# Optimization experiments

Hardware: AMD Instinct MI355X
Metric: run time of the kernel (lower is better)

Reference implementation:

```python
import jax, jax.numpy as jnp
import numpy as np

B, M, S, D, Q, H = 8, 8192, 128, 512, 32, 8
HD = D // H
LN_EPS = 1e-5


def setup_inputs() -> dict:
    key = jax.random.key(0)
    ks = jax.random.split(key, 12)
    inp = {
        "memory": jax.random.normal(ks[0], (B, M, D), dtype=jnp.float32),
        "context": jax.random.normal(ks[1], (B, S, D), dtype=jnp.float32),
        "memory_mask": jax.random.randint(ks[2], (B, M), 0, 2).astype(bool),
        # learned parameters
        "queries_param": jax.random.normal(ks[3], (Q, D), dtype=jnp.float32) * 0.02,
        "ctx_w": jax.random.normal(ks[4], (D, D), dtype=jnp.float32) / np.sqrt(D),
        "ctx_b": jnp.zeros((D,), dtype=jnp.float32),
        "in_w": jax.random.normal(ks[5], (3 * D, D), dtype=jnp.float32) / np.sqrt(D),
        "in_b": jnp.zeros((3 * D,), dtype=jnp.float32),
        "out_w": jax.random.normal(ks[6], (D, D), dtype=jnp.float32) / np.sqrt(D),
        "out_b": jnp.zeros((D,), dtype=jnp.float32),
        "ln_g": jnp.ones((D,), dtype=jnp.float32),
        "ln_b": jnp.zeros((D,), dtype=jnp.float32),
        "gate_w": jax.random.normal(ks[7], (Q, D), dtype=jnp.float32) / np.sqrt(D),
        "gate_b": jnp.zeros((Q,), dtype=jnp.float32),
    }
    return inp


def _forward(memory, context, memory_mask, queries_param, ctx_w, ctx_b,
             in_w, in_b, out_w, out_b, ln_g, ln_b, gate_w, gate_b):
    b = memory.shape[0]
    # pool context over sequence dim (rank-3 path)
    pooled = context.mean(axis=1)  # [B, D]
    # queries + projected context
    queries = queries_param[None, :, :] + (pooled @ ctx_w.T + ctx_b)[:, None, :]  # [B, Q, D]
    # MultiheadAttention in-projection
    wq, wk, wv = in_w[:D], in_w[D:2 * D], in_w[2 * D:]
    bq, bk, bv = in_b[:D], in_b[D:2 * D], in_b[2 * D:]
    qh = (queries @ wq.T + bq).reshape(b, Q, H, HD).transpose(0, 2, 1, 3)   # [B,H,Q,hd]
    kh = (memory @ wk.T + bk).reshape(b, M, H, HD).transpose(0, 2, 1, 3)    # [B,H,M,hd]
    vh = (memory @ wv.T + bv).reshape(b, M, H, HD).transpose(0, 2, 1, 3)    # [B,H,M,hd]
    scale = 1.0 / np.sqrt(HD)
    scores = jnp.einsum('bhqd,bhkd->bhqk', qh * scale, kh)                  # [B,H,Q,M]
    # key_padding_mask: True in memory_mask means valid; invalid -> -inf
    scores = jnp.where(memory_mask[:, None, None, :], scores, -jnp.inf)
    attn = jax.nn.softmax(scores, axis=-1)                                   # [B,H,Q,M]
    ctx_out = jnp.einsum('bhqk,bhkd->bhqd', attn, vh)
    ctx_out = ctx_out.transpose(0, 2, 1, 3).reshape(b, Q, D)
    readouts = ctx_out @ out_w.T + out_b                                     # [B,Q,D]
    attention = attn.mean(axis=1)                                            # [B,Q,M]
    gates = jax.nn.sigmoid(pooled @ gate_w.T + gate_b)                       # [B,Q]
    readouts = readouts * gates[:, :, None]
    mu = readouts.mean(axis=-1, keepdims=True)
    var = readouts.var(axis=-1, keepdims=True)
    readouts_norm = (readouts - mu) * jax.lax.rsqrt(var + LN_EPS) * ln_g + ln_b
    return readouts_norm, attention, gates, queries


def reference(memory, context, memory_mask, queries_param, ctx_w, ctx_b,
              in_w, in_b, out_w, out_b, ln_g, ln_b, gate_w, gate_b):
    return _forward(memory, context, memory_mask, queries_param, ctx_w, ctx_b,
                    in_w, in_b, out_w, out_b, ln_g, ln_b, gate_w, gate_b)
```

## Files before the change

### kernel.cpp

```cpp
#include <hip/hip_runtime.h>
#include <cstdint>

#define BB 8
#define MM 8192
#define SS 128
#define DD 512
#define QQ 32
#define HH 8
#define HDD 64
#define LN_EPS 1e-5f

typedef __bf16 bf16;
typedef _Float16 f16;
typedef __attribute__((ext_vector_type(8))) __bf16 bf16x8;
typedef __attribute__((ext_vector_type(4))) __bf16 bf16x4;
typedef __attribute__((ext_vector_type(8))) _Float16 f16x8;
typedef __attribute__((ext_vector_type(4))) float f32x4;

#define NEG_INF (-__builtin_inff())

__global__ __launch_bounds__(512) void k_front(const float* __restrict__ ctx,
                                               const float* __restrict__ ctx_w,
                                               const float* __restrict__ ctx_b,
                                               const float* __restrict__ qp,
                                               const float* __restrict__ gate_w,
                                               const float* __restrict__ gate_b,
                                               float* __restrict__ q_out,
                                               float* __restrict__ gates_out) {
    __shared__ float pl[DD];
    __shared__ float scratch[512];
    __shared__ float proj[64];
    int blk = blockIdx.x;
    int b = blk >> 3, js = blk & 7;
    int t = threadIdx.x;
    const float* p = ctx + (size_t)b * SS * DD + t;
    float s = 0.f;
#pragma unroll 8
    for (int i = 0; i < SS; i++) s += p[(size_t)i * DD];
    pl[t] = s * (1.0f / SS);
    __syncthreads();
    int r = js * 64 + (t & 63), ks = t >> 6;
    {
        const f32x4* wr = (const f32x4*)(ctx_w + (size_t)r * DD + ks * 64);
        const f32x4* pv = (const f32x4*)(pl + ks * 64);
        float a = 0.f;
#pragma unroll
        for (int k = 0; k < 16; k++) {
            f32x4 w = wr[k], pp = pv[k];
            a += w.x * pp.x + w.y * pp.y + w.z * pp.z + w.w * pp.w;
        }
        scratch[t] = a;
    }
    __syncthreads();
    if (t < 64) {
        float sum = ctx_b[js * 64 + t];
#pragma unroll
        for (int s8 = 0; s8 < 8; s8++) sum += scratch[t + 64 * s8];
        proj[t] = sum;
    }
    __syncthreads();
    int col = js * 64 + (t & 63);
    float pr = proj[t & 63];
#pragma unroll
    for (int qq = 0; qq < 4; qq++) {
        int q = (t >> 6) * 4 + qq;
        q_out[((size_t)(b * QQ + q)) * DD + col] = qp[q * DD + col] + pr;
    }
    if (js == 0 && t < QQ) {
        const f32x4* gw = (const f32x4*)(gate_w + (size_t)t * DD);
        const f32x4* pv = (const f32x4*)pl;
        float ga = 0.f;
#pragma unroll 8
        for (int k = 0; k < DD / 4; k++) {
            f32x4 w = gw[k], pp = pv[k];
            ga += w.x * pp.x + w.y * pp.y + w.z * pp.z + w.w * pp.w;
        }
        gates_out[b * QQ + t] = 1.0f / (1.0f + __expf(-(ga + gate_b[t])));
    }
}

__global__ __launch_bounds__(256) void k_qh(const float* __restrict__ q_in,
                                            const float* __restrict__ in_w,
                                            const float* __restrict__ in_b,
                                            float* __restrict__ qh) {
    __shared__ float qr[QQ * DD];
    int blk = blockIdx.x;
    int b = blk >> 3, js = blk & 7;
    int t = threadIdx.x;
    const f32x4* src = (const f32x4*)(q_in + (size_t)b * QQ * DD);
    f32x4* dst = (f32x4*)qr;
    for (int i = t; i < QQ * DD / 4; i += 256) dst[i] = src[i];
    __syncthreads();
    int j = js * 64 + (t & 63);
    int qg = t >> 6;
    const f32x4* wv = (const f32x4*)(in_w + (size_t)j * DD);
    float acc[8];
#pragma unroll
    for (int e = 0; e < 8; e++) acc[e] = 0.f;
    for (int k = 0; k < DD / 4; k++) {
        f32x4 w = wv[k];
#pragma unroll
        for (int e = 0; e < 8; e++) {
            f32x4 qq = ((const f32x4*)qr)[(qg * 8 + e) * (DD / 4) + k];
            acc[e] += w.x * qq.x + w.y * qq.y + w.z * qq.z + w.w * qq.w;
        }
    }
    float bias = in_b[j];
#pragma unroll
    for (int e = 0; e < 8; e++) {
        int q = qg * 8 + e;
        qh[((size_t)(b * QQ + q)) * DD + j] = 0.125f * (acc[e] + bias);
    }
}

__global__ void k_cvt(const float* __restrict__ src, bf16* __restrict__ dst, int n4) {
    int i = blockIdx.x * blockDim.x + threadIdx.x;
    if (i >= n4) return;
    f32x4 v = ((const f32x4*)src)[i];
    bf16x4 o;
    o.x = (bf16)v.x; o.y = (bf16)v.y; o.z = (bf16)v.z; o.w = (bf16)v.w;
    ((bf16x4*)dst)[i] = o;
}

#define GLOAD(gp, lp)                                                                   \
    __builtin_amdgcn_global_load_lds((const __attribute__((address_space(1))) void*)(gp), \
                                     (__attribute__((address_space(3))) void*)(lp), 16, 0, 0)

__global__ __launch_bounds__(512, 2) void k_gemm_kv(const bf16* __restrict__ A,
                                                    const bf16* __restrict__ Bw,
                                                    const float* __restrict__ in_b,
                                                    bf16* __restrict__ Kh,
                                                    bf16* __restrict__ Vt) {
    __shared__ __align__(16) bf16 sm[65536];
    const int tid = threadIdx.x;
    const int w = tid >> 6, l = tid & 63;
    const int wm = w >> 2, wn = w & 3;
    const int lq = l & 15, quad = l >> 4, lx = l & 7;
    const int lr = l >> 3, gc = (l & 7) ^ lr;
    const int sb = (w >> 1) * 8 + (w & 1) * 2;

    const int bid = blockIdx.x;
    const int swz = (bid & 7) * 128 + (bid >> 3);
    const int bm = swz >> 2, bn = swz & 3;

    const bf16* aPtr = A + (size_t)(bm * 256 + w * 8 + lr) * 512 + gc * 8;
    const bf16* bPtr = Bw + (size_t)(bn * 256 + sb * 8 + lr) * 512 + gc * 8;

#pragma unroll
    for (int p = 0; p < 4; p++) GLOAD(aPtr + p * 32768, sm + (p * 8 + w) * 512);
#pragma unroll
    for (int p = 0; p < 4; p++) {
        GLOAD(bPtr + ((p & 1) * 8 + (p >> 1) * 32) * 512,
              sm + 16384 + (sb + (p & 1) + (p >> 1) * 4) * 512);
        if (p == 1) __builtin_amdgcn_sched_barrier(0);
    }
    aPtr += 64;
    bPtr += 64;

    const f32x4 vzero = {0.f, 0.f, 0.f, 0.f};
    f32x4 acc[8][4];
#pragma unroll
    for (int i = 0; i < 8; i++)
#pragma unroll
        for (int j = 0; j < 4; j++) acc[i][j] = vzero;

#pragma unroll
    for (int T = 0; T < 8; T++) {
        bf16* Ab = sm + (T & 1) * 32768;
        bf16* Bb = Ab + 16384;
        bf16* AbN = sm + ((T + 1) & 1) * 32768;
        bf16* BbN = AbN + 16384;
        const bool pf = (T < 7);

        asm volatile("s_waitcnt vmcnt(2)" ::: "memory");
        __builtin_amdgcn_s_barrier();
        bf16x8 af[8][2], b01[2][2];
        {
            const int c0 = (quad ^ lx) << 3;
#pragma unroll
            for (int i = 0; i < 8; i++) {
                const bf16* rp = Ab + (wm * 128 + i * 16 + lq) * 64;
                af[i][0] = *(const bf16x8*)(rp + c0);
                af[i][1] = *(const bf16x8*)(rp + (c0 ^ 32));
            }
#pragma unroll
            for (int j = 0; j < 2; j++) {
                const bf16* rp = Bb + (wn * 64 + j * 16 + lq) * 64;
                b01[j][0] = *(const bf16x8*)(rp + c0);
                b01[j][1] = *(const bf16x8*)(rp + (c0 ^ 32));
            }
        }
        if (pf) {
#pragma unroll
            for (int p = 0; p < 4; p++) GLOAD(aPtr + p * 32768, AbN + (p * 8 + w) * 512);
            aPtr += 64;
        }
        __builtin_amdgcn_s_setprio(1);
#pragma unroll
        for (int i = 0; i < 8; i++)
#pragma unroll
            for (int j = 0; j < 2; j++) {
                acc[i][j] = __builtin_amdgcn_mfma_f32_16x16x32_bf16(af[i][0], b01[j][0], acc[i][j], 0, 0, 0);
                acc[i][j] = __builtin_amdgcn_mfma_f32_16x16x32_bf16(af[i][1], b01[j][1], acc[i][j], 0, 0, 0);
            }
        __builtin_amdgcn_s_setprio(0);

        if (pf) {
            asm volatile("s_waitcnt vmcnt(4)" ::: "memory");
        } else {
            asm volatile("s_waitcnt vmcnt(0)" ::: "memory");
        }
        __builtin_amdgcn_s_barrier();
        bf16x8 b23[2][2];
        {
            const int c0 = (quad ^ lx) << 3;
#pragma unroll
            for (int j = 0; j < 2; j++) {
                const bf16* rp = Bb + (wn * 64 + 32 + j * 16 + lq) * 64;
                b23[j][0] = *(const bf16x8*)(rp + c0);
                b23[j][1] = *(const bf16x8*)(rp + (c0 ^ 32));
            }
        }
        if (pf) {
#pragma unroll
            for (int p = 0; p < 4; p++) {
                GLOAD(bPtr + ((p & 1) * 8 + (p >> 1) * 32) * 512,
                      BbN + (sb + (p & 1) + (p >> 1) * 4) * 512);
                if (p == 1) __builtin_amdgcn_sched_barrier(0);
            }
            bPtr += 64;
        }
        __builtin_amdgcn_s_setprio(1);
#pragma unroll
        for (int i = 0; i < 8; i++)
#pragma unroll
            for (int j = 0; j < 2; j++) {
                acc[i][2 + j] = __builtin_amdgcn_mfma_f32_16x16x32_bf16(af[i][0], b23[j][0], acc[i][2 + j], 0, 0, 0);
                acc[i][2 + j] = __builtin_amdgcn_mfma_f32_16x16x32_bf16(af[i][1], b23[j][1], acc[i][2 + j], 0, 0, 0);
            }
        __builtin_amdgcn_s_setprio(0);
    }

    __syncthreads();
    const int qn_w = wn >> 1;
    bf16* qt = sm + (((wm << 1) | qn_w) * 16384);
    const bool isV = (bn >= 2);
    if (!isV) {
#pragma unroll
        for (int j = 0; j < 4; j++) {
            int cq = (wn & 1) * 64 + j * 16 + lq;
            float bias = in_b[512 + bn * 256 + qn_w * 128 + cq];
            int cc = cq >> 3, cl = cq & 7;
#pragma unroll
            for (int i = 0; i < 8; i++) {
                int rb = i * 16 + quad * 4;
#pragma unroll
                for (int t = 0; t < 4; t++) {
                    int r = rb + t;
                    qt[r * 128 + (((cc ^ (r & 15)) << 3) | cl)] = (bf16)(acc[i][j][t] + bias);
                }
            }
        }
        __syncthreads();
        for (int idx = tid; idx < 8192; idx += 512) {
            int qq2 = idx >> 11;
            int rr = (idx >> 4) & 127, ch2 = idx & 15;
            bf16x8 v = *(const bf16x8*)(sm + qq2 * 16384 + rr * 128 + ((ch2 ^ (rr & 15)) << 3));
            int m = bm * 256 + (qq2 >> 1) * 128 + rr;
            int cg = bn * 256 + (qq2 & 1) * 128 + ch2 * 8;
            int b = m >> 13, mloc = m & 8191;
            int h = cg >> 6, d = cg & 63;
            *(bf16x8*)(Kh + (((size_t)(b * 8 + h) * 8192 + mloc) << 6) + d) = v;
        }
    } else {
#pragma unroll
        for (int j = 0; j < 4; j++) {
            int cq = (wn & 1) * 64 + j * 16 + lq;
            float bias = in_b[512 + bn * 256 + qn_w * 128 + cq];
            int cs = cq & 15;
#pragma unroll
            for (int i = 0; i < 8; i++) {
                int rb = i * 16 + quad * 4;
#pragma unroll
                for (int t = 0; t < 4; t++) {
                    int r = rb + t;
                    qt[cq * 128 + ((((r >> 3) ^ cs) << 3) | (r & 7))] = (bf16)(acc[i][j][t] + bias);
                }
            }
        }
        __syncthreads();
        for (int idx = tid; idx < 8192; idx += 512) {
            int qq2 = idx >> 11;
            int cq = (idx >> 4) & 127, ch2 = idx & 15;
            bf16x8 v = *(const bf16x8*)(sm + qq2 * 16384 + cq * 128 + ((ch2 ^ (cq & 15)) << 3));
            int hd = (bn - 2) * 256 + (qq2 & 1) * 128 + cq;
            int m = bm * 256 + (qq2 >> 1) * 128 + ch2 * 8;
            int b = m >> 13, mloc = m & 8191;
            *(bf16x8*)(Vt + ((size_t)(b * 512 + hd)) * MM + mloc) = v;
        }
    }
}
#undef GLOAD

__global__ __launch_bounds__(256) void k_scores(const float* __restrict__ qh,
                                                const bf16* __restrict__ kvK,
                                                const int* __restrict__ mask,
                                                f16* __restrict__ s16,
                                                float* __restrict__ statsM,
                                                float* __restrict__ statsS) {
    __shared__ __align__(16) f16 tile[QQ * 528];
    __shared__ float smx[QQ][4];
    __shared__ float sse[QQ][4];
    __shared__ float qmax[QQ];
    int blk = blockIdx.x;
    int mt = blk & 15, h = (blk >> 4) & 7, b = blk >> 7;
    int tid = threadIdx.x, w = tid >> 6, l = tid & 63;
    int lq = l & 15, quad = l >> 4;
    int mbase = mt * 512 + w * 128;

    bf16x8 af[2][2];
#pragma unroll
    for (int i = 0; i < 2; i++)
#pragma unroll
        for (int s = 0; s < 2; s++) {
            const float* qp = qh + ((size_t)(b * QQ + i * 16 + lq)) * DD + h * 64 + s * 32 + quad * 8;
            f32x4 q0 = *(const f32x4*)qp;
            f32x4 q1 = *(const f32x4*)(qp + 4);
            bf16x8 v;
            v[0] = (bf16)q0.x; v[1] = (bf16)q0.y; v[2] = (bf16)q0.z; v[3] = (bf16)q0.w;
            v[4] = (bf16)q1.x; v[5] = (bf16)q1.y; v[6] = (bf16)q1.z; v[7] = (bf16)q1.w;
            af[i][s] = v;
        }

    const f32x4 vzero = {0.f, 0.f, 0.f, 0.f};
    f32x4 acc[2][8];
#pragma unroll
    for (int i = 0; i < 2; i++)
#pragma unroll
        for (int n = 0; n < 8; n++) acc[i][n] = vzero;

#pragma unroll
    for (int n = 0; n < 8; n++) {
        int m = mbase + n * 16 + lq;
        const bf16* kp = kvK + (((size_t)(b * HH + h) * MM + m) << 6) + quad * 8;
        bf16x8 b0 = *(const bf16x8*)kp;
        bf16x8 b1 = *(const bf16x8*)(kp + 32);
#pragma unroll
        for (int i = 0; i < 2; i++) {
            acc[i][n] = __builtin_amdgcn_mfma_f32_16x16x32_bf16(af[i][0], b0, acc[i][n], 0, 0, 0);
            acc[i][n] = __builtin_amdgcn_mfma_f32_16x16x32_bf16(af[i][1], b1, acc[i][n], 0, 0, 0);
        }
    }
#pragma unroll
    for (int n = 0; n < 8; n++) {
        int mv = mask[b * MM + mbase + n * 16 + lq];
        if (!mv) {
#pragma unroll
            for (int i = 0; i < 2; i++)
#pragma unroll
                for (int t = 0; t < 4; t++) acc[i][n][t] = NEG_INF;
        }
    }
    float mx[2][4];
#pragma unroll
    for (int i = 0; i < 2; i++)
#pragma unroll
        for (int t = 0; t < 4; t++) {
            float m = acc[i][0][t];
#pragma unroll
            for (int n = 1; n < 8; n++) m = fmaxf(m, acc[i][n][t]);
            mx[i][t] = m;
        }
#pragma unroll
    for (int off = 1; off < 16; off <<= 1)
#pragma unroll
        for (int i = 0; i < 2; i++)
#pragma unroll
            for (int t = 0; t < 4; t++) mx[i][t] = fmaxf(mx[i][t], __shfl_xor(mx[i][t], off, 64));
    if (lq == 0) {
#pragma unroll
        for (int i = 0; i < 2; i++)
#pragma unroll
            for (int t = 0; t < 4; t++) smx[i * 16 + quad * 4 + t][w] = mx[i][t];
    }
    __syncthreads();
    if (tid < QQ) qmax[tid] = fmaxf(fmaxf(smx[tid][0], smx[tid][1]), fmaxf(smx[tid][2], smx[tid][3]));
    __syncthreads();
    float se[2][4];
#pragma unroll
    for (int i = 0; i < 2; i++)
#pragma unroll
        for (int t = 0; t < 4; t++) {
            float qm = qmax[i * 16 + quad * 4 + t];
            float s = 0.f;
#pragma unroll
            for (int n = 0; n < 8; n++) s += __expf(acc[i][n][t] - qm);
            se[i][t] = s;
        }
#pragma unroll
    for (int off = 1; off < 16; off <<= 1)
#pragma unroll
        for (int i = 0; i < 2; i++)
#pragma unroll
            for (int t = 0; t < 4; t++) se[i][t] += __shfl_xor(se[i][t], off, 64);
    if (lq == 0) {
#pragma unroll
        for (int i = 0; i < 2; i++)
#pragma unroll
            for (int t = 0; t < 4; t++) sse[i * 16 + quad * 4 + t][w] = se[i][t];
    }
#pragma unroll
    for (int n = 0; n < 8; n++) {
        int mloc = w * 128 + n * 16 + lq;
#pragma unroll
        for (int i = 0; i < 2; i++)
#pragma unroll
            for (int t = 0; t < 4; t++)
                tile[(i * 16 + quad * 4 + t) * 528 + mloc] = (f16)acc[i][n][t];
    }
    __syncthreads();
    if (tid < QQ) {
        statsM[(size_t)blk * QQ + tid] = qmax[tid];
        statsS[(size_t)blk * QQ + tid] = sse[tid][0] + sse[tid][1] + sse[tid][2] + sse[tid][3];
    }
    for (int it = tid; it < 2048; it += 256) {
        int q = it >> 6, c = it & 63;
        f16x8 v = *(const f16x8*)(tile + q * 528 + c * 8);
        *(f16x8*)(s16 + ((size_t)((b * HH + h) * QQ + q)) * MM + mt * 512 + c * 8) = v;
    }
}

__global__ __launch_bounds__(256) void k_attn(const f16* __restrict__ s16,
                                              const float* __restrict__ statsM,
                                              const float* __restrict__ statsS,
                                              float* __restrict__ attn_out) {
    __shared__ float cM[128], cS[128], Mh[HH], iLh[HH];
    int blk = blockIdx.x;
    int ms = blk & 3, q = (blk >> 2) & 31, b = blk >> 7;
    int t = threadIdx.x;
    if (t < 128) {
        int h = t >> 4, c = t & 15;
        size_t sidx = (size_t)(((b * HH + h) * 16 + c)) * QQ + q;
        cM[t] = statsM[sidx];
        cS[t] = statsS[sidx];
    }
    __syncthreads();
    if (t < HH) {
        float M = NEG_INF;
#pragma unroll
        for (int c = 0; c < 16; c++) M = fmaxf(M, cM[t * 16 + c]);
        float L = 0.f;
#pragma unroll
        for (int c = 0; c < 16; c++) L += cS[t * 16 + c] * __expf(cM[t * 16 + c] - M);
        Mh[t] = M;
        iLh[t] = (1.0f / L) * (1.0f / HH);
    }
    __syncthreads();
    int m0 = ms * 2048 + t * 8;
    float am[8];
#pragma unroll
    for (int e = 0; e < 8; e++) am[e] = 0.f;
#pragma unroll
    for (int h = 0; h < HH; h++) {
        f16x8 v = *(const f16x8*)(s16 + ((size_t)((b * HH + h) * QQ + q)) * MM + m0);
        float M = Mh[h], iL = iLh[h];
#pragma unroll
        for (int e = 0; e < 8; e++) am[e] += __expf((float)v[e] - M) * iL;
    }
    float* ao = attn_out + (size_t)(b * QQ + q) * MM + m0;
    f32x4 o0 = {am[0], am[1], am[2], am[3]};
    f32x4 o1 = {am[4], am[5], am[6], am[7]};
    *(f32x4*)ao = o0;
    *(f32x4*)(ao + 4) = o1;
}

__global__ __launch_bounds__(256) void k_pv(const f16* __restrict__ s16,
                                            const float* __restrict__ statsM,
                                            const float* __restrict__ statsS,
                                            const bf16* __restrict__ Vt,
                                            float* __restrict__ ctxo_p) {
    __shared__ float ctile[QQ * HDD];
    __shared__ float Mq[QQ], iLq[QQ];
    int blk = blockIdx.x;
    int ck = blk & 7, h = (blk >> 3) & 7, b = blk >> 6;
    int t = threadIdx.x, w = t >> 6, l = t & 63;
    int lq = l & 15, quad = l >> 4;
    if (t < QQ) {
        const float* pM = statsM + (size_t)((b * HH + h) * 16) * QQ + t;
        const float* pS = statsS + (size_t)((b * HH + h) * 16) * QQ + t;
        float M = NEG_INF;
#pragma unroll
        for (int c = 0; c < 16; c++) M = fmaxf(M, pM[c * QQ]);
        float L = 0.f;
#pragma unroll
        for (int c = 0; c < 16; c++) L += pS[c * QQ] * __expf(pM[c * QQ] - M);
        Mq[t] = M;
        iLq[t] = 1.0f / L;
    }
    __syncthreads();
    int m0 = ck * 1024 + w * 256;

    const f16* P0 = s16 + ((size_t)((b * HH + h) * QQ + lq)) * MM + m0 + quad * 8;
    const f16* P1 = P0 + (size_t)16 * MM;
    const bf16* Vrow = Vt + ((size_t)((b * HH + h) * HDD + lq)) * MM + m0 + quad * 8;
    float M0 = Mq[lq], iL0 = iLq[lq];
    float M1 = Mq[16 + lq], iL1 = iLq[16 + lq];

    const f32x4 vzero = {0.f, 0.f, 0.f, 0.f};
    f32x4 acc[2][4];
#pragma unroll
    for (int i = 0; i < 2; i++)
#pragma unroll
        for (int j = 0; j < 4; j++) acc[i][j] = vzero;

#pragma unroll 2
    for (int ks = 0; ks < 256; ks += 32) {
        f16x8 r0 = *(const f16x8*)(P0 + ks);
        f16x8 r1 = *(const f16x8*)(P1 + ks);
        bf16x8 a0, a1;
#pragma unroll
        for (int e = 0; e < 8; e++) a0[e] = (bf16)(__expf((float)r0[e] - M0) * iL0);
#pragma unroll
        for (int e = 0; e < 8; e++) a1[e] = (bf16)(__expf((float)r1[e] - M1) * iL1);
        bf16x8 bv[4];
#pragma unroll
        for (int j = 0; j < 4; j++) bv[j] = *(const bf16x8*)(Vrow + (size_t)j * 16 * MM + ks);
#pragma unroll
        for (int j = 0; j < 4; j++) {
            acc[0][j] = __builtin_amdgcn_mfma_f32_16x16x32_bf16(a0, bv[j], acc[0][j], 0, 0, 0);
            acc[1][j] = __builtin_amdgcn_mfma_f32_16x16x32_bf16(a1, bv[j], acc[1][j], 0, 0, 0);
        }
    }
    for (int i = t; i < QQ * HDD; i += 256) ctile[i] = 0.f;
    __syncthreads();
#pragma unroll
    for (int i = 0; i < 2; i++)
#pragma unroll
        for (int j = 0; j < 4; j++)
#pragma unroll
            for (int tt = 0; tt < 4; tt++) {
                int q = i * 16 + quad * 4 + tt;
                int d = j * 16 + lq;
                atomicAdd(&ctile[q * HDD + d], acc[i][j][tt]);
            }
    __syncthreads();
    float* dst = ctxo_p + (size_t)ck * (BB * QQ * DD);
    for (int i = t; i < QQ * HDD; i += 256) {
        int q = i >> 6, d = i & 63;
        dst[((size_t)(b * QQ + q)) * DD + h * HDD + d] = ctile[i];
    }
}

__global__ __launch_bounds__(256) void k_outln(const float* __restrict__ ctxo_p,
                                               const float* __restrict__ out_w,
                                               const float* __restrict__ out_b,
                                               const float* __restrict__ gates,
                                               const float* __restrict__ ln_g,
                                               const float* __restrict__ ln_b,
                                               float* __restrict__ out0) {
    __shared__ float cr[DD];
    __shared__ float sred[4], sred2[4];
    int bq = blockIdx.x, t = threadIdx.x;
    float c0 = 0.f, c1 = 0.f;
#pragma unroll
    for (int c = 0; c < 8; c++) {
        const float* src = ctxo_p + (size_t)c * (BB * QQ * DD) + (size_t)bq * DD;
        c0 += src[t];
        c1 += src[t + 256];
    }
    cr[t] = c0;
    cr[t + 256] = c1;
    __syncthreads();
    float g = gates[bq];
    const f32x4* cv = (const f32x4*)cr;
    float r[2];
#pragma unroll
    for (int jj = 0; jj < 2; jj++) {
        int j = t + jj * 256;
        const f32x4* wv = (const f32x4*)(out_w + (size_t)j * DD);
        float acc = 0.f;
#pragma unroll 4
        for (int k = 0; k < DD / 4; k++) {
            f32x4 wq = wv[k], cq = cv[k];
            acc += wq.x * cq.x + wq.y * cq.y + wq.z * cq.z + wq.w * cq.w;
        }
        r[jj] = (acc + out_b[j]) * g;
    }
    float s1 = r[0] + r[1];
    float s2 = r[0] * r[0] + r[1] * r[1];
    for (int off = 32; off; off >>= 1) {
        s1 += __shfl_xor(s1, off, 64);
        s2 += __shfl_xor(s2, off, 64);
    }
    int wid = t >> 6;
    if ((t & 63) == 0) { sred[wid] = s1; sred2[wid] = s2; }
    __syncthreads();
    float S1 = sred[0] + sred[1] + sred[2] + sred[3];
    float S2 = sred2[0] + sred2[1] + sred2[2] + sred2[3];
    float mu = S1 * (1.0f / DD);
    float var = S2 * (1.0f / DD) - mu * mu;
    float rs = rsqrtf(var + LN_EPS);
#pragma unroll
    for (int jj = 0; jj < 2; jj++) {
        int j = t + jj * 256;
        out0[(size_t)bq * DD + j] = (r[jj] - mu) * rs * ln_g[j] + ln_b[j];
    }
}

extern "C" void kernel_launch(void* const* d_in, const int* in_sizes, int n_in,
                              void* d_out, int out_size, void* d_ws, size_t ws_size,
                              hipStream_t stream) {
    const float* memory  = (const float*)d_in[0];
    const float* context = (const float*)d_in[1];
    const int*   mask    = (const int*)d_in[2];
    const float* qp      = (const float*)d_in[3];
    const float* ctx_w   = (const float*)d_in[4];
    const float* ctx_b   = (const float*)d_in[5];
    const float* in_w    = (const float*)d_in[6];
    const float* in_b    = (const float*)d_in[7];
    const float* out_w   = (const float*)d_in[8];
    const float* out_b   = (const float*)d_in[9];
    const float* ln_g    = (const float*)d_in[10];
    const float* ln_b    = (const float*)d_in[11];
    const float* gate_w  = (const float*)d_in[12];
    const float* gate_b  = (const float*)d_in[13];

    float* out       = (float*)d_out;
    float* out_ln    = out;
    float* out_attn  = out + 131072;
    float* out_gates = out + 131072 + 2097152;
    float* out_q     = out_gates + 256;

    char* ws = (char*)d_ws;
    bf16*  memB   = (bf16*)ws;
    f16*   s16    = (f16*)ws;
    bf16*  kvK    = (bf16*)(ws + 67108864);
    bf16*  Vt     = (bf16*)(ws + 134217728);
    bf16*  kvwB   = (bf16*)(ws + 201326592);
    float* statsM = (float*)(ws + 201588736);
    float* statsS = (float*)(ws + 201719808);
    float* qh     = (float*)(ws + 202375168);
    float* ctxo_p = (float*)(ws + 202899456);

    k_front<<<64, 512, 0, stream>>>(context, ctx_w, ctx_b, qp, gate_w, gate_b, out_q, out_gates);
    k_qh<<<64, 256, 0, stream>>>(out_q, in_w, in_b, qh);
    k_cvt<<<32768, 256, 0, stream>>>(memory, memB, 8388608);
    k_cvt<<<512, 256, 0, stream>>>(in_w + 262144, kvwB, 131072);
    k_gemm_kv<<<1024, 512, 0, stream>>>(memB, kvwB, in_b, kvK, Vt);
    k_scores<<<1024, 256, 0, stream>>>(qh, kvK, mask, s16, statsM, statsS);
    k_attn<<<1024, 256, 0, stream>>>(s16, statsM, statsS, out_attn);
    k_pv<<<512, 256, 0, stream>>>(s16, statsM, statsS, Vt, ctxo_p);
    k_outln<<<BB * QQ, 256, 0, stream>>>(ctxo_p, out_w, out_b, out_gates, ln_g, ln_b, out_ln);
}
```

Measured before the change: 475.3 us.

## Fuse fp32-to-bf16 conversion of memory into the KV GEMM A-operand load

Drops the separate k_cvt pass over the 128 MB fp32 memory tensor. The KV GEMM now loads fp32 A tiles into registers, converts them to bf16 and writes them to LDS itself, software-pipelined two k-steps ahead, while B still uses direct global-to-LDS loads. This removes a full write and re-read of the bf16 copy. In exchange the GEMM reads twice as many bytes for A (once per N-tile block, four times in total), needs more registers at launch bounds 512x2, and adds VALU conversion work to the main loop.

```diff
diff --git a/kernel.cpp b/kernel.cpp
--- a/kernel.cpp
+++ b/kernel.cpp
@@ -125,8 +125,9 @@
 #define GLOAD(gp, lp)                                                                   \
     __builtin_amdgcn_global_load_lds((const __attribute__((address_space(1))) void*)(gp), \
                                      (__attribute__((address_space(3))) void*)(lp), 16, 0, 0)
-
-__global__ __launch_bounds__(512, 2) void k_gemm_kv(const bf16* __restrict__ A,
+#define SBAR0 __builtin_amdgcn_sched_barrier(0)
+
+__global__ __launch_bounds__(512, 2) void k_gemm_kv(const float* __restrict__ A32,
                                                     const bf16* __restrict__ Bw,
                                                     const float* __restrict__ in_b,
                                                     bf16* __restrict__ Kh,
@@ -143,26 +144,48 @@
     const int swz = (bid & 7) * 128 + (bid >> 3);
     const int bm = swz >> 2, bn = swz & 3;
 
-    const bf16* aPtr = A + (size_t)(bm * 256 + w * 8 + lr) * 512 + gc * 8;
-    const bf16* bPtr = Bw + (size_t)(bn * 256 + sb * 8 + lr) * 512 + gc * 8;
-
-#pragma unroll
-    for (int p = 0; p < 4; p++) GLOAD(aPtr + p * 32768, sm + (p * 8 + w) * 512);
-#pragma unroll
-    for (int p = 0; p < 4; p++) {
-        GLOAD(bPtr + ((p & 1) * 8 + (p >> 1) * 32) * 512,
-              sm + 16384 + (sb + (p & 1) + (p >> 1) * 4) * 512);
-        if (p == 1) __builtin_amdgcn_sched_barrier(0);
-    }
-    aPtr += 64;
-    bPtr += 64;
-
+    const float* aG = A32 + (size_t)(bm * 256 + w * 8 + lr) * 512 + (l & 7) * 8;
+    const int aWr = (w * 8 + lr) * 64 + gc * 8;
+    const bf16* bG = Bw + (size_t)(bn * 256 + sb * 8 + lr) * 512 + gc * 8;
+
+#define LOADA(ar, kk)                                                        \
+    _Pragma("unroll") for (int p = 0; p < 4; p++) {                          \
+        ar[p][0] = *(const f32x4*)(aG + (size_t)p * 32768 + (kk));           \
+        ar[p][1] = *(const f32x4*)(aG + (size_t)p * 32768 + (kk) + 4);       \
+    }
+#define WRITEA(buf, ar)                                                      \
+    _Pragma("unroll") for (int p = 0; p < 4; p++) {                          \
+        bf16x8 v_;                                                           \
+        v_[0] = (bf16)ar[p][0].x; v_[1] = (bf16)ar[p][0].y;                  \
+        v_[2] = (bf16)ar[p][0].z; v_[3] = (bf16)ar[p][0].w;                  \
+        v_[4] = (bf16)ar[p][1].x; v_[5] = (bf16)ar[p][1].y;                  \
+        v_[6] = (bf16)ar[p][1].z; v_[7] = (bf16)ar[p][1].w;                  \
+        *(bf16x8*)((buf) + aWr + p * 4096) = v_;                             \
+    }
+#define LOADB(buf, kk)                                                       \
+    _Pragma("unroll") for (int p = 0; p < 4; p++) {                          \
+        GLOAD(bG + (size_t)(((p & 1) * 8 + (p >> 1) * 32) * 512) + (kk),     \
+              (buf) + (sb + (p & 1) + (p >> 1) * 4) * 512);                  \
+    }
+
+    f32x4 aRegA[4][2], aRegB[4][2];
     const f32x4 vzero = {0.f, 0.f, 0.f, 0.f};
     f32x4 acc[8][4];
 #pragma unroll
     for (int i = 0; i < 8; i++)
 #pragma unroll
         for (int j = 0; j < 4; j++) acc[i][j] = vzero;
+
+    LOADA(aRegA, 0);
+    SBAR0;
+    LOADB(sm + 16384, 0);
+    SBAR0;
+    asm volatile("s_waitcnt vmcnt(4)" ::: "memory");
+    WRITEA(sm, aRegA);
+    LOADA(aRegB, 64);
+    SBAR0;
+    asm volatile("s_waitcnt vmcnt(8) lgkmcnt(0)" ::: "memory");
+    __builtin_amdgcn_s_barrier();
 
 #pragma unroll
     for (int T = 0; T < 8; T++) {
@@ -170,31 +193,23 @@
         bf16* Bb = Ab + 16384;
         bf16* AbN = sm + ((T + 1) & 1) * 32768;
         bf16* BbN = AbN + 16384;
-        const bool pf = (T < 7);
-
-        asm volatile("s_waitcnt vmcnt(2)" ::: "memory");
-        __builtin_amdgcn_s_barrier();
+        const int c0 = (quad ^ lx) << 3;
+
         bf16x8 af[8][2], b01[2][2];
-        {
-            const int c0 = (quad ^ lx) << 3;
-#pragma unroll
-            for (int i = 0; i < 8; i++) {
-                const bf16* rp = Ab + (wm * 128 + i * 16 + lq) * 64;
-                af[i][0] = *(const bf16x8*)(rp + c0);
-                af[i][1] = *(const bf16x8*)(rp + (c0 ^ 32));
-            }
-#pragma unroll
-            for (int j = 0; j < 2; j++) {
-                const bf16* rp = Bb + (wn * 64 + j * 16 + lq) * 64;
-                b01[j][0] = *(const bf16x8*)(rp + c0);
-                b01[j][1] = *(const bf16x8*)(rp + (c0 ^ 32));
-            }
-        }
-        if (pf) {
-#pragma unroll
-            for (int p = 0; p < 4; p++) GLOAD(aPtr + p * 32768, AbN + (p * 8 + w) * 512);
-            aPtr += 64;
-        }
+#pragma unroll
+        for (int i = 0; i < 8; i++) {
+            const bf16* rp = Ab + (wm * 128 + i * 16 + lq) * 64;
+            af[i][0] = *(const bf16x8*)(rp + c0);
+            af[i][1] = *(const bf16x8*)(rp + (c0 ^ 32));
+        }
+#pragma unroll
+        for (int j = 0; j < 2; j++) {
+            const bf16* rp = Bb + (wn * 64 + j * 16 + lq) * 64;
+            b01[j][0] = *(const bf16x8*)(rp + c0);
+            b01[j][1] = *(const bf16x8*)(rp + (c0 ^ 32));
+        }
+        asm volatile("s_waitcnt lgkmcnt(0)" ::: "memory");
+        SBAR0;
         __builtin_amdgcn_s_setprio(1);
 #pragma unroll
         for (int i = 0; i < 8; i++)
@@ -205,31 +220,28 @@
             }
         __builtin_amdgcn_s_setprio(0);
 
-        if (pf) {
+        if (T < 7) {
+            LOADB(BbN, (T + 1) * 64);
+            SBAR0;
             asm volatile("s_waitcnt vmcnt(4)" ::: "memory");
-        } else {
-            asm volatile("s_waitcnt vmcnt(0)" ::: "memory");
-        }
-        __builtin_amdgcn_s_barrier();
+            if ((T & 1) == 0) {
+                WRITEA(AbN, aRegB);
+                if (T < 6) LOADA(aRegA, (T + 2) * 64);
+            } else {
+                WRITEA(AbN, aRegA);
+                if (T < 6) LOADA(aRegB, (T + 2) * 64);
+            }
+            SBAR0;
+        }
         bf16x8 b23[2][2];
-        {
-            const int c0 = (quad ^ lx) << 3;
-#pragma unroll
-            for (int j = 0; j < 2; j++) {
-                const bf16* rp = Bb + (wn * 64 + 32 + j * 16 + lq) * 64;
-                b23[j][0] = *(const bf16x8*)(rp + c0);
-                b23[j][1] = *(const bf16x8*)(rp + (c0 ^ 32));
-            }
-        }
-        if (pf) {
-#pragma unroll
-            for (int p = 0; p < 4; p++) {
-                GLOAD(bPtr + ((p & 1) * 8 + (p >> 1) * 32) * 512,
-                      BbN + (sb + (p & 1) + (p >> 1) * 4) * 512);
-                if (p == 1) __builtin_amdgcn_sched_barrier(0);
-            }
-            bPtr += 64;
-        }
+#pragma unroll
+        for (int j = 0; j < 2; j++) {
+            const bf16* rp = Bb + (wn * 64 + 32 + j * 16 + lq) * 64;
+            b23[j][0] = *(const bf16x8*)(rp + c0);
+            b23[j][1] = *(const bf16x8*)(rp + (c0 ^ 32));
+        }
+        asm volatile("s_waitcnt lgkmcnt(0)" ::: "memory");
+        SBAR0;
         __builtin_amdgcn_s_setprio(1);
 #pragma unroll
         for (int i = 0; i < 8; i++)
@@ -239,7 +251,17 @@
                 acc[i][2 + j] = __builtin_amdgcn_mfma_f32_16x16x32_bf16(af[i][1], b23[j][1], acc[i][2 + j], 0, 0, 0);
             }
         __builtin_amdgcn_s_setprio(0);
-    }
+        if (T < 6) {
+            asm volatile("s_waitcnt vmcnt(8)" ::: "memory");
+            __builtin_amdgcn_s_barrier();
+        } else if (T == 6) {
+            asm volatile("s_waitcnt vmcnt(0)" ::: "memory");
+            __builtin_amdgcn_s_barrier();
+        }
+    }
+#undef LOADA
+#undef WRITEA
+#undef LOADB
 
     __syncthreads();
     const int qn_w = wn >> 1;
@@ -301,6 +323,7 @@
     }
 }
 #undef GLOAD
+#undef SBAR0
 
 __global__ __launch_bounds__(256) void k_scores(const float* __restrict__ qh,
                                                 const bf16* __restrict__ kvK,
@@ -632,7 +655,6 @@
     float* out_q     = out_gates + 256;
 
     char* ws = (char*)d_ws;
-    bf16*  memB   = (bf16*)ws;
     f16*   s16    = (f16*)ws;
     bf16*  kvK    = (bf16*)(ws + 67108864);
     bf16*  Vt     = (bf16*)(ws + 134217728);
@@ -644,9 +666,8 @@
 
     k_front<<<64, 512, 0, stream>>>(context, ctx_w, ctx_b, qp, gate_w, gate_b, out_q, out_gates);
     k_qh<<<64, 256, 0, stream>>>(out_q, in_w, in_b, qh);
-    k_cvt<<<32768, 256, 0, stream>>>(memory, memB, 8388608);
     k_cvt<<<512, 256, 0, stream>>>(in_w + 262144, kvwB, 131072);
-    k_gemm_kv<<<1024, 512, 0, stream>>>(memB, kvwB, in_b, kvK, Vt);
+    k_gemm_kv<<<1024, 512, 0, stream>>>(memory, kvwB, in_b, kvK, Vt);
     k_scores<<<1024, 256, 0, stream>>>(qh, kvK, mask, s16, statsM, statsS);
     k_attn<<<1024, 256, 0, stream>>>(s16, statsM, statsS, out_attn);
     k_pv<<<512, 256, 0, stream>>>(s16, statsM, statsS, Vt, ctxo_p);
```

Measured after the change: 693.3 us. 1.46x slower.

## Fuse P·V into the scores kernel with chunk-local softmax and rescale later

Applied to the files above, without the earlier changes.

The separate P·V kernel is removed. The scores kernel now computes exp(s - chunk_max) in place, stores these local probabilities as f16, and multiplies them against V (now stored as f16) with MFMA to write per-chunk partial context vectors. The output kernel and the attention-mean kernel rescale each chunk by exp(chunk_max - global_max)/L instead of recomputing exp per element. This removes a kernel launch and the re-read of the score matrix for P·V. In exchange it adds per-chunk partial buffers, more LDS and work in the scores kernel, and f16 precision for both V and the probabilities.

```diff
diff --git a/kernel.cpp b/kernel.cpp
--- a/kernel.cpp
+++ b/kernel.cpp
@@ -130,7 +130,7 @@
                                                     const bf16* __restrict__ Bw,
                                                     const float* __restrict__ in_b,
                                                     bf16* __restrict__ Kh,
-                                                    bf16* __restrict__ Vt) {
+                                                    f16* __restrict__ Vt) {
     __shared__ __align__(16) bf16 sm[65536];
     const int tid = threadIdx.x;
     const int w = tid >> 6, l = tid & 63;
@@ -273,6 +273,7 @@
             *(bf16x8*)(Kh + (((size_t)(b * 8 + h) * 8192 + mloc) << 6) + d) = v;
         }
     } else {
+        f16* qth = (f16*)qt;
 #pragma unroll
         for (int j = 0; j < 4; j++) {
             int cq = (wn & 1) * 64 + j * 16 + lq;
@@ -284,7 +285,7 @@
 #pragma unroll
                 for (int t = 0; t < 4; t++) {
                     int r = rb + t;
-                    qt[cq * 128 + ((((r >> 3) ^ cs) << 3) | (r & 7))] = (bf16)(acc[i][j][t] + bias);
+                    qth[cq * 128 + ((((r >> 3) ^ cs) << 3) | (r & 7))] = (f16)(acc[i][j][t] + bias);
                 }
             }
         }
@@ -292,11 +293,11 @@
         for (int idx = tid; idx < 8192; idx += 512) {
             int qq2 = idx >> 11;
             int cq = (idx >> 4) & 127, ch2 = idx & 15;
-            bf16x8 v = *(const bf16x8*)(sm + qq2 * 16384 + cq * 128 + ((ch2 ^ (cq & 15)) << 3));
+            f16x8 v = *(const f16x8*)((const f16*)sm + qq2 * 16384 + cq * 128 + ((ch2 ^ (cq & 15)) << 3));
             int hd = (bn - 2) * 256 + (qq2 & 1) * 128 + cq;
             int m = bm * 256 + (qq2 >> 1) * 128 + ch2 * 8;
             int b = m >> 13, mloc = m & 8191;
-            *(bf16x8*)(Vt + ((size_t)(b * 512 + hd)) * MM + mloc) = v;
+            *(f16x8*)(Vt + ((size_t)(b * 512 + hd)) * MM + mloc) = v;
         }
     }
 }
@@ -304,11 +305,14 @@
 
 __global__ __launch_bounds__(256) void k_scores(const float* __restrict__ qh,
                                                 const bf16* __restrict__ kvK,
+                                                const f16* __restrict__ Vt,
                                                 const int* __restrict__ mask,
                                                 f16* __restrict__ s16,
                                                 float* __restrict__ statsM,
-                                                float* __restrict__ statsS) {
-    __shared__ __align__(16) f16 tile[QQ * 528];
+                                                float* __restrict__ statsS,
+                                                float* __restrict__ cp) {
+    __shared__ __align__(16) f16 tile[QQ * 520];
+    __shared__ float ctile[QQ * HDD];
     __shared__ float smx[QQ][4];
     __shared__ float sse[QQ][4];
     __shared__ float qmax[QQ];
@@ -318,6 +322,8 @@
     int lq = l & 15, quad = l >> 4;
     int mbase = mt * 512 + w * 128;
 
+    for (int i = tid; i < QQ * HDD; i += 256) ctile[i] = 0.f;
+
     bf16x8 af[2][2];
 #pragma unroll
     for (int i = 0; i < 2; i++)
@@ -391,10 +397,15 @@
     for (int i = 0; i < 2; i++)
 #pragma unroll
         for (int t = 0; t < 4; t++) {
-            float qm = qmax[i * 16 + quad * 4 + t];
+            int qrow = i * 16 + quad * 4 + t;
+            float qm = qmax[qrow];
             float s = 0.f;
 #pragma unroll
-            for (int n = 0; n < 8; n++) s += __expf(acc[i][n][t] - qm);
+            for (int n = 0; n < 8; n++) {
+                float p = __expf(acc[i][n][t] - qm);
+                s += p;
+                tile[qrow * 520 + w * 128 + n * 16 + lq] = (f16)p;
+            }
             se[i][t] = s;
         }
 #pragma unroll
@@ -408,15 +419,6 @@
         for (int i = 0; i < 2; i++)
 #pragma unroll
             for (int t = 0; t < 4; t++) sse[i * 16 + quad * 4 + t][w] = se[i][t];
-    }
-#pragma unroll
-    for (int n = 0; n < 8; n++) {
-        int mloc = w * 128 + n * 16 + lq;
-#pragma unroll
-        for (int i = 0; i < 2; i++)
-#pragma unroll
-            for (int t = 0; t < 4; t++)
-                tile[(i * 16 + quad * 4 + t) * 528 + mloc] = (f16)acc[i][n][t];
     }
     __syncthreads();
     if (tid < QQ) {
@@ -425,8 +427,42 @@
     }
     for (int it = tid; it < 2048; it += 256) {
         int q = it >> 6, c = it & 63;
-        f16x8 v = *(const f16x8*)(tile + q * 528 + c * 8);
+        f16x8 v = *(const f16x8*)(tile + q * 520 + c * 8);
         *(f16x8*)(s16 + ((size_t)((b * HH + h) * QQ + q)) * MM + mt * 512 + c * 8) = v;
+    }
+    f32x4 acc2[2][4];
+#pragma unroll
+    for (int i = 0; i < 2; i++)
+#pragma unroll
+        for (int j = 0; j < 4; j++) acc2[i][j] = vzero;
+    const f16* vbase = Vt + ((size_t)(b * 512 + h * 64 + lq)) * MM + mbase + quad * 8;
+#pragma unroll
+    for (int ks = 0; ks < 4; ks++) {
+        f16x8 pb[2];
+        pb[0] = *(const f16x8*)(tile + lq * 520 + w * 128 + ks * 32 + quad * 8);
+        pb[1] = *(const f16x8*)(tile + (16 + lq) * 520 + w * 128 + ks * 32 + quad * 8);
+        f16x8 va[4];
+#pragma unroll
+        for (int j = 0; j < 4; j++)
+            va[j] = *(const f16x8*)(vbase + (size_t)(j * 16) * MM + ks * 32);
+#pragma unroll
+        for (int j = 0; j < 4; j++) {
+            acc2[0][j] = __builtin_amdgcn_mfma_f32_16x16x32_f16(va[j], pb[0], acc2[0][j], 0, 0, 0);
+            acc2[1][j] = __builtin_amdgcn_mfma_f32_16x16x32_f16(va[j], pb[1], acc2[1][j], 0, 0, 0);
+        }
+    }
+#pragma unroll
+    for (int i = 0; i < 2; i++)
+#pragma unroll
+        for (int j = 0; j < 4; j++)
+#pragma unroll
+            for (int t = 0; t < 4; t++)
+                atomicAdd(&ctile[(i * 16 + lq) * HDD + j * 16 + quad * 4 + t], acc2[i][j][t]);
+    __syncthreads();
+    {
+        f32x4* cd = (f32x4*)(cp + ((size_t)((b * HH + h) * 16 + mt)) * (QQ * HDD));
+        const f32x4* cs = (const f32x4*)ctile;
+        for (int i = tid; i < QQ * HDD / 4; i += 256) cd[i] = cs[i];
     }
 }
 
@@ -434,7 +470,7 @@
                                               const float* __restrict__ statsM,
                                               const float* __restrict__ statsS,
                                               float* __restrict__ attn_out) {
-    __shared__ float cM[128], cS[128], Mh[HH], iLh[HH];
+    __shared__ float cM[128], cS[128], Mh[HH], iLh[HH], wgt[128];
     int blk = blockIdx.x;
     int ms = blk & 3, q = (blk >> 2) & 31, b = blk >> 7;
     int t = threadIdx.x;
@@ -456,16 +492,19 @@
         iLh[t] = (1.0f / L) * (1.0f / HH);
     }
     __syncthreads();
+    if (t < 128) wgt[t] = __expf(cM[t] - Mh[t >> 4]) * iLh[t >> 4];
+    __syncthreads();
     int m0 = ms * 2048 + t * 8;
+    int cloc = ms * 4 + (t >> 6);
     float am[8];
 #pragma unroll
     for (int e = 0; e < 8; e++) am[e] = 0.f;
 #pragma unroll
     for (int h = 0; h < HH; h++) {
         f16x8 v = *(const f16x8*)(s16 + ((size_t)((b * HH + h) * QQ + q)) * MM + m0);
-        float M = Mh[h], iL = iLh[h];
-#pragma unroll
-        for (int e = 0; e < 8; e++) am[e] += __expf((float)v[e] - M) * iL;
+        float wc = wgt[h * 16 + cloc];
+#pragma unroll
+        for (int e = 0; e < 8; e++) am[e] += (float)v[e] * wc;
     }
     float* ao = attn_out + (size_t)(b * QQ + q) * MM + m0;
     f32x4 o0 = {am[0], am[1], am[2], am[3]};
@@ -474,84 +513,9 @@
     *(f32x4*)(ao + 4) = o1;
 }
 
-__global__ __launch_bounds__(256) void k_pv(const f16* __restrict__ s16,
-                                            const float* __restrict__ statsM,
-                                            const float* __restrict__ statsS,
-                                            const bf16* __restrict__ Vt,
-                                            float* __restrict__ ctxo_p) {
-    __shared__ float ctile[QQ * HDD];
-    __shared__ float Mq[QQ], iLq[QQ];
-    int blk = blockIdx.x;
-    int ck = blk & 7, h = (blk >> 3) & 7, b = blk >> 6;
-    int t = threadIdx.x, w = t >> 6, l = t & 63;
-    int lq = l & 15, quad = l >> 4;
-    if (t < QQ) {
-        const float* pM = statsM + (size_t)((b * HH + h) * 16) * QQ + t;
-        const float* pS = statsS + (size_t)((b * HH + h) * 16) * QQ + t;
-        float M = NEG_INF;
-#pragma unroll
-        for (int c = 0; c < 16; c++) M = fmaxf(M, pM[c * QQ]);
-        float L = 0.f;
-#pragma unroll
-        for (int c = 0; c < 16; c++) L += pS[c * QQ] * __expf(pM[c * QQ] - M);
-        Mq[t] = M;
-        iLq[t] = 1.0f / L;
-    }
-    __syncthreads();
-    int m0 = ck * 1024 + w * 256;
-
-    const f16* P0 = s16 + ((size_t)((b * HH + h) * QQ + lq)) * MM + m0 + quad * 8;
-    const f16* P1 = P0 + (size_t)16 * MM;
-    const bf16* Vrow = Vt + ((size_t)((b * HH + h) * HDD + lq)) * MM + m0 + quad * 8;
-    float M0 = Mq[lq], iL0 = iLq[lq];
-    float M1 = Mq[16 + lq], iL1 = iLq[16 + lq];
-
-    const f32x4 vzero = {0.f, 0.f, 0.f, 0.f};
-    f32x4 acc[2][4];
-#pragma unroll
-    for (int i = 0; i < 2; i++)
-#pragma unroll
-        for (int j = 0; j < 4; j++) acc[i][j] = vzero;
-
-#pragma unroll 2
-    for (int ks = 0; ks < 256; ks += 32) {
-        f16x8 r0 = *(const f16x8*)(P0 + ks);
-        f16x8 r1 = *(const f16x8*)(P1 + ks);
-        bf16x8 a0, a1;
-#pragma unroll
-        for (int e = 0; e < 8; e++) a0[e] = (bf16)(__expf((float)r0[e] - M0) * iL0);
-#pragma unroll
-        for (int e = 0; e < 8; e++) a1[e] = (bf16)(__expf((float)r1[e] - M1) * iL1);
-        bf16x8 bv[4];
-#pragma unroll
-        for (int j = 0; j < 4; j++) bv[j] = *(const bf16x8*)(Vrow + (size_t)j * 16 * MM + ks);
-#pragma unroll
-        for (int j = 0; j < 4; j++) {
-            acc[0][j] = __builtin_amdgcn_mfma_f32_16x16x32_bf16(a0, bv[j], acc[0][j], 0, 0, 0);
-            acc[1][j] = __builtin_amdgcn_mfma_f32_16x16x32_bf16(a1, bv[j], acc[1][j], 0, 0, 0);
-        }
-    }
-    for (int i = t; i < QQ * HDD; i += 256) ctile[i] = 0.f;
-    __syncthreads();
-#pragma unroll
-    for (int i = 0; i < 2; i++)
-#pragma unroll
-        for (int j = 0; j < 4; j++)
-#pragma unroll
-            for (int tt = 0; tt < 4; tt++) {
-                int q = i * 16 + quad * 4 + tt;
-                int d = j * 16 + lq;
-                atomicAdd(&ctile[q * HDD + d], acc[i][j][tt]);
-            }
-    __syncthreads();
-    float* dst = ctxo_p + (size_t)ck * (BB * QQ * DD);
-    for (int i = t; i < QQ * HDD; i += 256) {
-        int q = i >> 6, d = i & 63;
-        dst[((size_t)(b * QQ + q)) * DD + h * HDD + d] = ctile[i];
-    }
-}
-
-__global__ __launch_bounds__(256) void k_outln(const float* __restrict__ ctxo_p,
+__global__ __launch_bounds__(256) void k_outln(const float* __restrict__ cp,
+                                               const float* __restrict__ statsM,
+                                               const float* __restrict__ statsS,
                                                const float* __restrict__ out_w,
                                                const float* __restrict__ out_b,
                                                const float* __restrict__ gates,
@@ -559,14 +523,39 @@
                                                const float* __restrict__ ln_b,
                                                float* __restrict__ out0) {
     __shared__ float cr[DD];
+    __shared__ float cM[128], cS[128], sMh[8], siL[8], wgt[128];
     __shared__ float sred[4], sred2[4];
     int bq = blockIdx.x, t = threadIdx.x;
+    int b = bq >> 5, q = bq & 31;
+    if (t < 128) {
+        int h = t >> 4, c = t & 15;
+        size_t sidx = (size_t)(((b * HH + h) * 16 + c)) * QQ + q;
+        cM[t] = statsM[sidx];
+        cS[t] = statsS[sidx];
+    }
+    __syncthreads();
+    if (t < 8) {
+        float M = NEG_INF;
+#pragma unroll
+        for (int c = 0; c < 16; c++) M = fmaxf(M, cM[t * 16 + c]);
+        float L = 0.f;
+#pragma unroll
+        for (int c = 0; c < 16; c++) L += cS[t * 16 + c] * __expf(cM[t * 16 + c] - M);
+        sMh[t] = M;
+        siL[t] = 1.0f / L;
+    }
+    __syncthreads();
+    if (t < 128) wgt[t] = __expf(cM[t] - sMh[t >> 4]) * siL[t >> 4];
+    __syncthreads();
+    int h0 = t >> 6, h1 = h0 + 4;
+    int dl = t & 63;
+    const float* cp0 = cp + ((size_t)((b * HH + h0) * 16)) * (QQ * HDD) + q * HDD + dl;
+    const float* cp1 = cp + ((size_t)((b * HH + h1) * 16)) * (QQ * HDD) + q * HDD + dl;
     float c0 = 0.f, c1 = 0.f;
 #pragma unroll
-    for (int c = 0; c < 8; c++) {
-        const float* src = ctxo_p + (size_t)c * (BB * QQ * DD) + (size_t)bq * DD;
-        c0 += src[t];
-        c1 += src[t + 256];
+    for (int c = 0; c < 16; c++) {
+        c0 += cp0[(size_t)c * (QQ * HDD)] * wgt[h0 * 16 + c];
+        c1 += cp1[(size_t)c * (QQ * HDD)] * wgt[h1 * 16 + c];
     }
     cr[t] = c0;
     cr[t + 256] = c1;
@@ -634,21 +623,20 @@
     char* ws = (char*)d_ws;
     bf16*  memB   = (bf16*)ws;
     f16*   s16    = (f16*)ws;
+    float* cp     = (float*)(ws + 35651584);
     bf16*  kvK    = (bf16*)(ws + 67108864);
-    bf16*  Vt     = (bf16*)(ws + 134217728);
+    f16*   Vt     = (f16*)(ws + 134217728);
     bf16*  kvwB   = (bf16*)(ws + 201326592);
     float* statsM = (float*)(ws + 201588736);
     float* statsS = (float*)(ws + 201719808);
     float* qh     = (float*)(ws + 202375168);
-    float* ctxo_p = (float*)(ws + 202899456);
 
     k_front<<<64, 512, 0, stream>>>(context, ctx_w, ctx_b, qp, gate_w, gate_b, out_q, out_gates);
     k_qh<<<64, 256, 0, stream>>>(out_q, in_w, in_b, qh);
     k_cvt<<<32768, 256, 0, stream>>>(memory, memB, 8388608);
     k_cvt<<<512, 256, 0, stream>>>(in_w + 262144, kvwB, 131072);
     k_gemm_kv<<<1024, 512, 0, stream>>>(memB, kvwB, in_b, kvK, Vt);
-    k_scores<<<1024, 256, 0, stream>>>(qh, kvK, mask, s16, statsM, statsS);
+    k_scores<<<1024, 256, 0, stream>>>(qh, kvK, Vt, mask, s16, statsM, statsS, cp);
     k_attn<<<1024, 256, 0, stream>>>(s16, statsM, statsS, out_attn);
-    k_pv<<<512, 256, 0, stream>>>(s16, statsM, statsS, Vt, ctxo_p);
-    k_outln<<<BB * QQ, 256, 0, stream>>>(ctxo_p, out_w, out_b, out_gates, ln_g, ln_b, out_ln);
-}
+    k_outln<<<BB * QQ, 256, 0, stream>>>(cp, statsM, statsS, out_w, out_b, out_gates, ln_g, ln_b, out_ln);
+}
```

Result: no change. 478.4 us (+0.7%).
